# Kernel optimization log

Hardware: AMD Instinct MI355X
Metric: run time of the kernel (lower is better)

The kernel has to match this reference:

```python
import jax, jax.numpy as jnp
import numpy as np

B, D, H = 131072, 1024, 128
ALL_PERMS = jnp.array([[0, 1, 2], [0, 2, 1], [1, 0, 2],
                       [1, 2, 0], [2, 0, 1], [2, 1, 0]], dtype=jnp.int32)


def setup_inputs() -> dict:
    key = jax.random.key(0)
    ks = jax.random.split(key, 10)
    inp_dim = D + 12  # d_model + 9 (state) + 3 (round one-hot)
    seq_embed = jax.random.normal(ks[0], (B, D), jnp.float32)
    freq = jax.random.uniform(ks[1], (B, 3), jnp.float32)
    pres = (jax.random.uniform(ks[2], (B, 3)) < 0.5).astype(jnp.float32)
    round_mask = (jax.random.uniform(ks[3], (B, 3)) < 0.5).astype(jnp.float32)
    perm_idx = jax.random.randint(ks[4], (B,), 0, 6, jnp.int32)
    W1 = jax.random.normal(ks[5], (inp_dim, H), jnp.float32) / np.sqrt(inp_dim).astype(np.float32)
    b1 = jnp.zeros((H,), jnp.float32)
    W2 = jax.random.normal(ks[6], (H, H), jnp.float32) / np.sqrt(H).astype(np.float32)
    b2 = jnp.zeros((H,), jnp.float32)
    W3 = jax.random.normal(ks[7], (H, 2), jnp.float32) / np.sqrt(H).astype(np.float32)
    b3 = jnp.zeros((2,), jnp.float32)
    return {"seq_embed": seq_embed, "freq": freq, "pres": pres,
            "round_mask": round_mask, "perm_idx": perm_idx,
            "W1": W1, "b1": b1, "W2": W2, "b2": b2, "W3": W3, "b3": b3}


def reference(seq_embed, freq, pres, round_mask, perm_idx, W1, b1, W2, b2, W3, b3):
    b = seq_embed.shape[0]
    dt = seq_embed.dtype
    perms = ALL_PERMS[perm_idx]                      # [B,3] round order per sample
    state = jnp.zeros((b, 9), dt)                    # 3 slots x [freq, pres, decoded]
    dec_f = jnp.zeros((b, 3), dt)
    dec_p = jnp.zeros((b, 3), dt)
    loss_sum = jnp.zeros((), dt)
    n_masked = jnp.zeros((), dt)
    ones_b = jnp.ones((b,), dt)
    for step in range(3):                            # fixed 3-step unroll (as original)
        ridx = perms[:, step]                        # [B]
        oh = jax.nn.one_hot(ridx, 3, dtype=dt)       # [B,3]
        gt_f = jnp.sum(freq * oh, axis=1)            # gather via one-hot
        gt_p = jnp.sum(pres * oh, axis=1)
        m = jnp.sum(round_mask * oh, axis=1)
        inp = jnp.concatenate([seq_embed, state, oh], axis=1)  # [B, D+12]
        h = jax.nn.gelu(inp @ W1 + b1, approximate=False)
        h = jax.nn.gelu(h @ W2 + b2, approximate=False)
        pred = h @ W3 + b3                           # [B,2]
        pf, z = pred[:, 0], pred[:, 1]
        fl = jnp.square(pf - gt_f) * m
        # sigmoid_cross_entropy_with_logits, numerically stable
        pl = (jnp.maximum(z, 0.0) - z * gt_p + jnp.log1p(jnp.exp(-jnp.abs(z)))) * m
        loss_sum = loss_sum + jnp.sum(fl + pl)
        n_masked = n_masked + jnp.sum(m)
        act_f = jnp.where(m > 0.5, pf, gt_f)
        act_p = jnp.where(m > 0.5, jax.nn.sigmoid(z), gt_p)
        new_vals = jnp.stack([act_f, act_p, ones_b], axis=1)   # [B,3]
        # scatter new_vals into slot ridx of state
        state3 = state.reshape(b, 3, 3)
        state = (state3 * (1.0 - oh)[:, :, None]
                 + new_vals[:, None, :] * oh[:, :, None]).reshape(b, 9)
        dec_f = dec_f * (1.0 - oh) + act_f[:, None] * oh
        dec_p = dec_p * (1.0 - oh) + act_p[:, None] * oh
    autoreg_loss = loss_sum / (n_masked + 1e-8)
    return autoreg_loss, dec_f, dec_p
```

## Files before the change

kernel.cpp:

```cpp
#include <hip/hip_runtime.h>
#include <math.h>

#define DDIM 1024
#define HDIM 128

typedef float  f32x4  __attribute__((ext_vector_type(4)));
typedef __bf16 bf16x8 __attribute__((ext_vector_type(8)));

union BF2U { __bf16 h; ushort u; };

__constant__ int c_perms[6][3] = {{0,1,2},{0,2,1},{1,0,2},{1,2,0},{2,0,1},{2,1,0}};

__device__ __forceinline__ ushort f2bf(float f){
    BF2U c; c.h = (__bf16)f; return c.u;
}
__device__ __forceinline__ float gelu_fast(float x){
    float a = fabsf(x) * 0.70710678118654752f;
    float t = __builtin_amdgcn_rcpf(fmaf(0.3275911f, a, 1.0f));
    float p = t * fmaf(t, fmaf(t, fmaf(t, fmaf(t, 1.061405429f, -1.453152027f),
                 1.421413741f), -0.284496736f), 0.254829592f);
    float y = 1.0f - p * __expf(-a * a);
    float er = copysignf(y, x);
    return 0.5f * x * (1.0f + er);
}

__global__ __launch_bounds__(256) void k0_prep(const float* __restrict__ W1,
                                               const float* __restrict__ W2,
                                               ushort* __restrict__ w1s,
                                               ushort* __restrict__ w2t)
{
    int i = blockIdx.x * 256 + threadIdx.x;
    if (i < DDIM * HDIM) {
        int t = i >> 12, rem = i & 4095;
        int n = rem >> 5, kk = rem & 31;
        int k = t * 32 + kk;
        w1s[i] = f2bf(W1[(size_t)k * HDIM + n]);
    } else if (i < DDIM * HDIM + HDIM * HDIM) {
        int j = i - DDIM * HDIM;
        int k = j >> 7, n = j & 127;
        ushort b = f2bf(W2[(size_t)k * HDIM + n]);
        size_t off = (size_t)n * 256 + (size_t)(((k * 2) ^ ((n & 7) << 4)));
        w2t[off >> 1] = b;
    }
}

__global__ __launch_bounds__(256, 3) void kf_fused(
    const float* __restrict__ seq,
    const ushort* __restrict__ w1s,
    const ushort* __restrict__ w2t,
    const float* __restrict__ freq,
    const float* __restrict__ pres,
    const float* __restrict__ rmask,
    const int*   __restrict__ pidx,
    const float* __restrict__ W1,
    const float* __restrict__ b1,
    const float* __restrict__ b2,
    const float* __restrict__ W3,
    const float* __restrict__ b3,
    float* __restrict__ dec_f,
    float* __restrict__ dec_p,
    float* __restrict__ partials)
{
    __shared__ __align__(16) char lds[52768];
    const int t = threadIdx.x;
    const int wid = t >> 6, lane = t & 63;
    const int g = lane >> 4, ln = lane & 15;
    const size_t row0 = (size_t)blockIdx.x * 64;

    const int srow  = wid * 8 + (lane >> 3);
    const int scolb = ((lane & 7) * 16) ^ ((lane >> 3) << 4);
    const int sldsw = wid * 1024;
    const int blane = lane * 16;

#define STAGE(BUF, TT) do { \
    _Pragma("unroll") \
    for (int j_ = 0; j_ < 2; ++j_) { \
        const char* ga_ = (const char*)(seq + (row0 + j_ * 32 + srow) * DDIM + (TT) * 32) + scolb; \
        char* la_ = lds + (BUF) * 8192 + j_ * 4096 + sldsw; \
        __builtin_amdgcn_global_load_lds((const __attribute__((address_space(1))) void*)ga_, \
                                         (__attribute__((address_space(3))) void*)la_, 16, 0, 0); \
    } \
    _Pragma("unroll") \
    for (int i_ = 0; i_ < 2; ++i_) { \
        const char* gb_ = (const char*)w1s + (size_t)(TT) * 8192 + i_ * 4096 + sldsw + blane; \
        char* lb_ = lds + 24576 + (BUF) * 8192 + i_ * 4096 + sldsw; \
        __builtin_amdgcn_global_load_lds((const __attribute__((address_space(1))) void*)gb_, \
                                         (__attribute__((address_space(3))) void*)lb_, 16, 0, 0); \
    } } while (0)

#define COMPUTE(BUF) do { \
    bf16x8 af; \
    { \
        const int p_ = wid * 16 + ln; \
        const int sw_ = (p_ & 7) << 4; \
        f32x4 x0 = *reinterpret_cast<const f32x4*>(lds + (BUF) * 8192 + p_ * 128 + ((g * 32 +  0) ^ sw_)); \
        f32x4 x1 = *reinterpret_cast<const f32x4*>(lds + (BUF) * 8192 + p_ * 128 + ((g * 32 + 16) ^ sw_)); \
        af[0] = (__bf16)x0[0]; af[1] = (__bf16)x0[1]; \
        af[2] = (__bf16)x0[2]; af[3] = (__bf16)x0[3]; \
        af[4] = (__bf16)x1[0]; af[5] = (__bf16)x1[1]; \
        af[6] = (__bf16)x1[2]; af[7] = (__bf16)x1[3]; \
    } \
    const ushort* btile = reinterpret_cast<const ushort*>(lds + 24576 + (BUF) * 8192); \
    _Pragma("unroll") \
    for (int nf_ = 0; nf_ < 8; ++nf_) { \
        bf16x8 bb = *reinterpret_cast<const bf16x8*>(btile + nf_ * 512 + ln * 32 + g * 8); \
        acc[nf_] = __builtin_amdgcn_mfma_f32_16x16x32_bf16(af, bb, acc[nf_], 0, 0, 0); \
    } } while (0)

#define WAITBAR(N) do { \
    asm volatile("s_waitcnt vmcnt(" #N ")" ::: "memory"); \
    __builtin_amdgcn_sched_barrier(0); \
    __builtin_amdgcn_s_barrier(); \
    __builtin_amdgcn_sched_barrier(0); } while (0)

    f32x4 acc[8];
#pragma unroll
    for (int n = 0; n < 8; ++n) acc[n] = (f32x4){0.f, 0.f, 0.f, 0.f};

    STAGE(0, 0);
    STAGE(1, 1);
    int cur = 0, nxt2 = 2;
    for (int tt = 0; tt < 30; ++tt) {
        WAITBAR(4);
        STAGE(nxt2, tt + 2);
        COMPUTE(cur);
        cur  = (cur  == 2) ? 0 : cur  + 1;
        nxt2 = (nxt2 == 2) ? 0 : nxt2 + 1;
    }
    WAITBAR(4);
    COMPUTE(cur);
    cur = (cur == 2) ? 0 : cur + 1;
    WAITBAR(0);
    COMPUTE(cur);
#undef WAITBAR
#undef COMPUTE
#undef STAGE

    __syncthreads();

    {
        float b1v[8];
#pragma unroll
        for (int nf = 0; nf < 8; ++nf) b1v[nf] = b1[nf * 16 + ln];
#pragma unroll
        for (int nf = 0; nf < 8; ++nf)
#pragma unroll
            for (int r = 0; r < 4; ++r) {
                int row = wid * 16 + g * 4 + r;
                int colb = (nf * 32 + ln * 2) ^ ((row & 7) << 4);
                *reinterpret_cast<ushort*>(lds + row * 256 + colb) = f2bf(acc[nf][r] + b1v[nf]);
            }
    }
#pragma unroll
    for (int i = 0; i < 8; ++i) {
        const char* gs = (const char*)w2t + i * 4096 + sldsw + blane;
        char* ds = lds + 16384 + i * 4096 + sldsw;
        __builtin_amdgcn_global_load_lds((const __attribute__((address_space(1))) void*)gs,
                                         (__attribute__((address_space(3))) void*)ds, 16, 0, 0);
    }
    {
        ushort* W1eh = (ushort*)(lds + 49152);
        for (int i = t; i < 12 * 128; i += 256)
            W1eh[i] = f2bf(W1[(size_t)(DDIM + (i >> 7)) * HDIM + (i & 127)]);
    }
    __syncthreads();

    const char*   W2s  = lds + 16384;
    const ushort* W1eh = (const ushort*)(lds + 49152);
    float* stl   = (float*)(lds + 52224 + wid * 128);
    float* lossw = (float*)(lds + 52736 + wid * 8);

    float b2v[8], w30[8], w31[8];
#pragma unroll
    for (int nf = 0; nf < 8; ++nf) {
        b2v[nf] = b2[nf * 16 + ln];
        w30[nf] = W3[(nf * 16 + ln) * 2 + 0];
        w31[nf] = W3[(nf * 16 + ln) * 2 + 1];
    }
    const float b30 = b3[0], b31 = b3[1];
    const bool owner = (ln < 4);
    float lossAcc = 0.f, maskAcc = 0.f;

    {
        const int prow = wid * 16 + ln;
        const size_t R_h = row0 + prow;
        const int pidx_h = pidx[R_h];

        float scon[32];
        {
            const int swzr = (ln & 7) << 4;
#pragma unroll
            for (int ks = 0; ks < 4; ++ks) {
                bf16x8 v = *reinterpret_cast<const bf16x8*>(lds + prow * 256 + ((ks * 64 + g * 16) ^ swzr));
#pragma unroll
                for (int j = 0; j < 8; ++j) scon[ks * 8 + j] = (float)v[j];
            }
        }
        const int rloc = g * 4 + ln;
        const size_t R_own = row0 + wid * 16 + rloc;
        int pio = 0;
        float ffo[3] = {0,0,0}, ppo[3] = {0,0,0}, mmo[3] = {0,0,0};
        if (owner) {
            pio = pidx[R_own];
#pragma unroll
            for (int q = 0; q < 3; ++q) {
                ffo[q] = freq[R_own * 3 + q];
                ppo[q] = pres[R_own * 3 + q];
                mmo[q] = rmask[R_own * 3 + q];
            }
        }

        for (int s = 0; s < 3; ++s) {
            const int ridx_h = c_perms[pidx_h][s];
            bf16x8 afr[4];
#pragma unroll
            for (int ks = 0; ks < 4; ++ks) {
                bf16x8 ov = *reinterpret_cast<const bf16x8*>(W1eh + (9 + ridx_h) * 128 + ks * 32 + g * 8);
#pragma unroll
                for (int j = 0; j < 8; ++j)
                    afr[ks][j] = (__bf16)gelu_fast(scon[ks * 8 + j] + (float)ov[j]);
            }
            f32x4 acc2[8];
#pragma unroll
            for (int nf = 0; nf < 8; ++nf) acc2[nf] = (f32x4){0.f, 0.f, 0.f, 0.f};
            __builtin_amdgcn_s_setprio(1);
#pragma unroll
            for (int ks = 0; ks < 4; ++ks) {
#pragma unroll
                for (int nf = 0; nf < 8; ++nf) {
                    const int n = nf * 16 + ln;
                    bf16x8 bb = *reinterpret_cast<const bf16x8*>(W2s + n * 256 + ((ks * 64 + g * 16) ^ ((n & 7) << 4)));
                    acc2[nf] = __builtin_amdgcn_mfma_f32_16x16x32_bf16(afr[ks], bb, acc2[nf], 0, 0, 0);
                }
            }
            __builtin_amdgcn_s_setprio(0);
            float p0[4] = {0, 0, 0, 0}, p1[4] = {0, 0, 0, 0};
#pragma unroll
            for (int nf = 0; nf < 8; ++nf) {
#pragma unroll
                for (int r = 0; r < 4; ++r) {
                    float h2 = gelu_fast(acc2[nf][r] + b2v[nf]);
                    p0[r] += h2 * w30[nf];
                    p1[r] += h2 * w31[nf];
                }
            }
#pragma unroll
            for (int mk = 1; mk < 16; mk <<= 1) {
#pragma unroll
                for (int r = 0; r < 4; ++r) {
                    p0[r] += __shfl_xor(p0[r], mk);
                    p1[r] += __shfl_xor(p1[r], mk);
                }
            }
            if (owner) {
                const int ridx_o = c_perms[pio][s];
                float pf = ((ln == 0) ? p0[0] : (ln == 1) ? p0[1] : (ln == 2) ? p0[2] : p0[3]) + b30;
                float z  = ((ln == 0) ? p1[0] : (ln == 1) ? p1[1] : (ln == 2) ? p1[2] : p1[3]) + b31;
                float gt_f = (ridx_o == 0) ? ffo[0] : (ridx_o == 1) ? ffo[1] : ffo[2];
                float gt_p = (ridx_o == 0) ? ppo[0] : (ridx_o == 1) ? ppo[1] : ppo[2];
                float m    = (ridx_o == 0) ? mmo[0] : (ridx_o == 1) ? mmo[1] : mmo[2];
                float d = pf - gt_f;
                float pl = (fmaxf(z, 0.f) - z * gt_p + __logf(1.0f + __expf(-fabsf(z)))) * m;
                lossAcc += d * d * m + pl;
                maskAcc += m;
                bool msk = m > 0.5f;
                float act_f = msk ? pf : gt_f;
                float act_p = msk ? __builtin_amdgcn_rcpf(1.f + __expf(-z)) : gt_p;
                stl[rloc * 2 + 0] = act_f;
                stl[rloc * 2 + 1] = act_p;
                dec_f[R_own * 3 + ridx_o] = act_f;
                dec_p[R_own * 3 + ridx_o] = act_p;
            }
            if (s < 2) {
                float af_ = stl[ln * 2 + 0];
                float ap_ = stl[ln * 2 + 1];
                const int c0 = g * 8;
#pragma unroll
                for (int ks = 0; ks < 4; ++ks) {
                    const int cc = ks * 32 + c0;
                    bf16x8 a0 = *reinterpret_cast<const bf16x8*>(W1eh + (ridx_h * 3 + 0) * 128 + cc);
                    bf16x8 b0 = *reinterpret_cast<const bf16x8*>(W1eh + (ridx_h * 3 + 1) * 128 + cc);
                    bf16x8 c0v = *reinterpret_cast<const bf16x8*>(W1eh + (ridx_h * 3 + 2) * 128 + cc);
#pragma unroll
                    for (int j = 0; j < 8; ++j)
                        scon[ks * 8 + j] += af_ * (float)a0[j] + ap_ * (float)b0[j] + (float)c0v[j];
                }
            }
        }
    }
#pragma unroll
    for (int mk = 1; mk < 64; mk <<= 1) {
        lossAcc += __shfl_xor(lossAcc, mk);
        maskAcc += __shfl_xor(maskAcc, mk);
    }
    if (lane == 0) { lossw[0] = lossAcc; lossw[1] = maskAcc; }
    __syncthreads();
    if (t == 0) {
        float ls = 0.f, ms = 0.f;
#pragma unroll
        for (int w = 0; w < 4; ++w) {
            const float* lw = (const float*)(lds + 52736 + w * 8);
            ls += lw[0]; ms += lw[1];
        }
        partials[2 * (size_t)blockIdx.x]     = ls;
        partials[2 * (size_t)blockIdx.x + 1] = ms;
    }
}

__global__ __launch_bounds__(256) void k3_reduce(const float* __restrict__ partials,
                                                 int nb, float* __restrict__ out)
{
    __shared__ float sl[256], sm[256];
    int t = threadIdx.x;
    float ls = 0.f, ms = 0.f;
    for (int i = t; i < nb; i += 256) { ls += partials[2 * i]; ms += partials[2 * i + 1]; }
    sl[t] = ls; sm[t] = ms;
    __syncthreads();
    for (int s = 128; s > 0; s >>= 1) {
        if (t < s) { sl[t] += sl[t + s]; sm[t] += sm[t + s]; }
        __syncthreads();
    }
    if (t == 0) out[0] = sl[0] / (sm[0] + 1e-8f);
}

extern "C" void kernel_launch(void* const* d_in, const int* in_sizes, int n_in,
                              void* d_out, int out_size, void* d_ws, size_t ws_size,
                              hipStream_t stream) {
    const float* seq   = (const float*)d_in[0];
    const float* freq  = (const float*)d_in[1];
    const float* pres  = (const float*)d_in[2];
    const float* rmask = (const float*)d_in[3];
    const int*   pidx  = (const int*)d_in[4];
    const float* W1    = (const float*)d_in[5];
    const float* b1    = (const float*)d_in[6];
    const float* W2    = (const float*)d_in[7];
    const float* b2    = (const float*)d_in[8];
    const float* W3    = (const float*)d_in[9];
    const float* b3    = (const float*)d_in[10];

    int B = in_sizes[4];
    float* out   = (float*)d_out;
    float* dec_f = out + 1;
    float* dec_p = out + 1 + (size_t)B * 3;

    char* ws = (char*)d_ws;
    float*  partials = (float*)ws;
    ushort* w1s  = (ushort*)(ws + 16384);
    ushort* w2t  = (ushort*)(ws + 16384 + 262144);

    int nblk = B / 64;
    k0_prep<<<(DDIM * HDIM + HDIM * HDIM + 255) / 256, 256, 0, stream>>>(W1, W2, w1s, w2t);
    kf_fused<<<nblk, 256, 0, stream>>>(seq, w1s, w2t, freq, pres, rmask, pidx,
                                       W1, b1, b2, W3, b3, dec_f, dec_p, partials);
    k3_reduce<<<1, 256, 0, stream>>>(partials, nblk, out);
}
```

Baseline: 174.5 us.

## Switch layer-1 GEMM to 64-wide K tiles with double buffering

The K tile for the first GEMM grows from 32 to 64 and the triple-buffered pipeline becomes a double-buffered one. Each iteration now waits for all outstanding loads, then issues the next stage before computing. This halves the number of barrier iterations and lets each wave issue larger loads. The cost is more LDS per block (64KB), which lowers the launch-bounds occupancy target from 3 to 2 blocks, and a shallower prefetch depth that can expose memory latency.

```diff
diff --git a/kernel.cpp b/kernel.cpp
--- a/kernel.cpp
+++ b/kernel.cpp
@@ -44,7 +44,7 @@
     }
 }
 
-__global__ __launch_bounds__(256, 3) void kf_fused(
+__global__ __launch_bounds__(256, 2) void kf_fused(
     const float* __restrict__ seq,
     const ushort* __restrict__ w1s,
     const ushort* __restrict__ w2t,
@@ -61,54 +61,57 @@
     float* __restrict__ dec_p,
     float* __restrict__ partials)
 {
-    __shared__ __align__(16) char lds[52768];
+    __shared__ __align__(16) char lds[65536];
     const int t = threadIdx.x;
     const int wid = t >> 6, lane = t & 63;
     const int g = lane >> 4, ln = lane & 15;
     const size_t row0 = (size_t)blockIdx.x * 64;
 
-    const int srow  = wid * 8 + (lane >> 3);
-    const int scolb = ((lane & 7) * 16) ^ ((lane >> 3) << 4);
-    const int sldsw = wid * 1024;
-    const int blane = lane * 16;
+    const int srow2  = wid * 4 + (lane >> 4);
+    const int scolb2 = ((lane & 15) * 16) ^ ((srow2 & 7) << 4);
+    const int sldsw  = wid * 1024;
+    const int blane  = lane * 16;
 
 #define STAGE(BUF, TT) do { \
     _Pragma("unroll") \
-    for (int j_ = 0; j_ < 2; ++j_) { \
-        const char* ga_ = (const char*)(seq + (row0 + j_ * 32 + srow) * DDIM + (TT) * 32) + scolb; \
-        char* la_ = lds + (BUF) * 8192 + j_ * 4096 + sldsw; \
+    for (int j_ = 0; j_ < 4; ++j_) { \
+        const char* ga_ = (const char*)(seq + (row0 + j_ * 16 + srow2) * DDIM + (TT) * 64) + scolb2; \
+        char* la_ = lds + (BUF) * 16384 + j_ * 4096 + sldsw; \
         __builtin_amdgcn_global_load_lds((const __attribute__((address_space(1))) void*)ga_, \
                                          (__attribute__((address_space(3))) void*)la_, 16, 0, 0); \
     } \
     _Pragma("unroll") \
-    for (int i_ = 0; i_ < 2; ++i_) { \
-        const char* gb_ = (const char*)w1s + (size_t)(TT) * 8192 + i_ * 4096 + sldsw + blane; \
-        char* lb_ = lds + 24576 + (BUF) * 8192 + i_ * 4096 + sldsw; \
+    for (int i_ = 0; i_ < 4; ++i_) { \
+        const char* gb_ = (const char*)w1s + (size_t)(TT) * 16384 + i_ * 4096 + sldsw + blane; \
+        char* lb_ = lds + 32768 + (BUF) * 16384 + i_ * 4096 + sldsw; \
         __builtin_amdgcn_global_load_lds((const __attribute__((address_space(1))) void*)gb_, \
                                          (__attribute__((address_space(3))) void*)lb_, 16, 0, 0); \
     } } while (0)
 
 #define COMPUTE(BUF) do { \
-    bf16x8 af; \
-    { \
-        const int p_ = wid * 16 + ln; \
-        const int sw_ = (p_ & 7) << 4; \
-        f32x4 x0 = *reinterpret_cast<const f32x4*>(lds + (BUF) * 8192 + p_ * 128 + ((g * 32 +  0) ^ sw_)); \
-        f32x4 x1 = *reinterpret_cast<const f32x4*>(lds + (BUF) * 8192 + p_ * 128 + ((g * 32 + 16) ^ sw_)); \
+    const int p_ = wid * 16 + ln; \
+    const int sw_ = (p_ & 7) << 4; \
+    const char* ab_ = lds + (BUF) * 16384 + p_ * 256; \
+    const ushort* bt_ = reinterpret_cast<const ushort*>(lds + 32768 + (BUF) * 16384); \
+    _Pragma("unroll") \
+    for (int h_ = 0; h_ < 2; ++h_) { \
+        bf16x8 af; \
+        f32x4 x0 = *reinterpret_cast<const f32x4*>(ab_ + ((h_ * 128 + g * 32 +  0) ^ sw_)); \
+        f32x4 x1 = *reinterpret_cast<const f32x4*>(ab_ + ((h_ * 128 + g * 32 + 16) ^ sw_)); \
         af[0] = (__bf16)x0[0]; af[1] = (__bf16)x0[1]; \
         af[2] = (__bf16)x0[2]; af[3] = (__bf16)x0[3]; \
         af[4] = (__bf16)x1[0]; af[5] = (__bf16)x1[1]; \
         af[6] = (__bf16)x1[2]; af[7] = (__bf16)x1[3]; \
-    } \
-    const ushort* btile = reinterpret_cast<const ushort*>(lds + 24576 + (BUF) * 8192); \
-    _Pragma("unroll") \
-    for (int nf_ = 0; nf_ < 8; ++nf_) { \
-        bf16x8 bb = *reinterpret_cast<const bf16x8*>(btile + nf_ * 512 + ln * 32 + g * 8); \
-        acc[nf_] = __builtin_amdgcn_mfma_f32_16x16x32_bf16(af, bb, acc[nf_], 0, 0, 0); \
+        const ushort* bh_ = bt_ + h_ * 4096; \
+        _Pragma("unroll") \
+        for (int nf_ = 0; nf_ < 8; ++nf_) { \
+            bf16x8 bb = *reinterpret_cast<const bf16x8*>(bh_ + nf_ * 512 + ln * 32 + g * 8); \
+            acc[nf_] = __builtin_amdgcn_mfma_f32_16x16x32_bf16(af, bb, acc[nf_], 0, 0, 0); \
+        } \
     } } while (0)
 
-#define WAITBAR(N) do { \
-    asm volatile("s_waitcnt vmcnt(" #N ")" ::: "memory"); \
+#define WAITBAR0 do { \
+    asm volatile("s_waitcnt vmcnt(0)" ::: "memory"); \
     __builtin_amdgcn_sched_barrier(0); \
     __builtin_amdgcn_s_barrier(); \
     __builtin_amdgcn_sched_barrier(0); } while (0)
@@ -118,21 +121,12 @@
     for (int n = 0; n < 8; ++n) acc[n] = (f32x4){0.f, 0.f, 0.f, 0.f};
 
     STAGE(0, 0);
-    STAGE(1, 1);
-    int cur = 0, nxt2 = 2;
-    for (int tt = 0; tt < 30; ++tt) {
-        WAITBAR(4);
-        STAGE(nxt2, tt + 2);
-        COMPUTE(cur);
-        cur  = (cur  == 2) ? 0 : cur  + 1;
-        nxt2 = (nxt2 == 2) ? 0 : nxt2 + 1;
-    }
-    WAITBAR(4);
-    COMPUTE(cur);
-    cur = (cur == 2) ? 0 : cur + 1;
-    WAITBAR(0);
-    COMPUTE(cur);
-#undef WAITBAR
+    for (int tt = 0; tt < 16; ++tt) {
+        WAITBAR0;
+        if (tt + 1 < 16) STAGE((tt + 1) & 1, tt + 1);
+        COMPUTE(tt & 1);
+    }
+#undef WAITBAR0
 #undef COMPUTE
 #undef STAGE
 
```

Result: slower. 188.1 us (+7.8%).
